# Performance work log

Hardware: AMD Instinct MI355X
Metric: run time of the kernel (lower is better)

Reference implementation:

```python
import jax, jax.numpy as jnp
import numpy as np

N, S, D, H = 4, 2048, 1024, 16
DH = D // H  # 64


def setup_inputs() -> dict:
    key = jax.random.key(0)
    ks = jax.random.split(key, 7)
    return {
        "sequences": jax.random.normal(ks[0], (N, S, D), dtype=jnp.float32),
        "Wq": jax.random.normal(ks[1], (H, DH, DH), dtype=jnp.float32) * (1.0 / np.sqrt(DH)),
        "bq": jax.random.normal(ks[2], (H, DH), dtype=jnp.float32) * 0.02,
        "Wk": jax.random.normal(ks[3], (H, DH, DH), dtype=jnp.float32) * (1.0 / np.sqrt(DH)),
        "bk": jax.random.normal(ks[4], (H, DH), dtype=jnp.float32) * 0.02,
        "Wv": jax.random.normal(ks[5], (H, DH, DH), dtype=jnp.float32) * (1.0 / np.sqrt(DH)),
        "bv": jax.random.normal(ks[6], (H, DH), dtype=jnp.float32) * 0.02,
    }


def reference(sequences, Wq, bq, Wk, bk, Wv, bv):
    n, s, d = sequences.shape
    # Each head h only sees its own slice of the embedding (block-diagonal proj)
    x = sequences.reshape(n, s, H, DH)  # (N, S, H, DH)
    q = jnp.einsum('nshd,hde->nshe', x, Wq) + bq  # (N, S, H, DH)
    k = jnp.einsum('nshd,hde->nshe', x, Wk) + bk
    v = jnp.einsum('nshd,hde->nshe', x, Wv) + bv
    scores = jnp.einsum('nqhd,nkhd->nhqk', q, k) / jnp.sqrt(jnp.float32(DH))
    attn = jax.nn.softmax(scores, axis=-1)  # (N, H, S, S)
    out = jnp.einsum('nhqk,nkhd->nqhd', attn, v)  # (N, S, H, DH)
    return out.reshape(n, s, d)  # hstack of heads == concat on last dim
```

## Files before the change

kernel.cpp:

```cpp
#include <hip/hip_runtime.h>
#include <hip/hip_bf16.h>

#define NB 4
#define SLEN 2048
#define DMODEL 1024
#define NH 16
#define DH 64

using f32x4  = __attribute__((ext_vector_type(4))) float;
using f32x8  = __attribute__((ext_vector_type(8))) float;
using f32x16 = __attribute__((ext_vector_type(16))) float;
using bf16x8 = __attribute__((ext_vector_type(8))) short;
using u32x4  = __attribute__((ext_vector_type(4))) unsigned int;

__device__ __forceinline__ unsigned short f2bf(float f) {
    unsigned int u = __float_as_uint(f);
    u += 0x7FFFu + ((u >> 16) & 1u);
    return (unsigned short)(u >> 16);
}

__device__ __forceinline__ float fast_exp2(float x) {
    float r;
    asm("v_exp_f32 %0, %1" : "=v"(r) : "v"(x));
    return r;
}

__device__ __forceinline__ unsigned cvtpk(float lo, float hi) {
    unsigned r;
    asm("v_cvt_pk_bf16_f32 %0, %1, %2" : "=v"(r) : "v"(lo), "v"(hi));
    return r;
}

__device__ __forceinline__ void permswap(unsigned& a, unsigned& b) {
    asm("v_permlane32_swap_b32 %0, %1" : "+v"(a), "+v"(b));
}

#define QSCALE 0.18033688011112042f

__global__ __launch_bounds__(256) void qkv_proj_kernel(
    const float* __restrict__ seq,
    const float* __restrict__ Wq, const float* __restrict__ bq,
    const float* __restrict__ Wk, const float* __restrict__ bk,
    const float* __restrict__ Wv, const float* __restrict__ bv,
    unsigned short* __restrict__ Qb,
    unsigned short* __restrict__ Kb,
    unsigned short* __restrict__ Vt)
{
    const int bid  = blockIdx.x;
    const int nh   = bid >> 5;
    const int tile = bid & 31;
    const int h = nh & 15;
    const int n = nh >> 4;
    const int t0 = tile * 64;
    const int tid = threadIdx.x;
    const int w  = tid >> 6;
    const int l  = tid & 63;
    const int g  = l >> 4;
    const int ln = l & 15;

    __shared__ unsigned short wt[3][64 * 72];

    {
        const float* Wsrc0 = Wq + h * 4096;
        const float* Wsrc1 = Wk + h * 4096;
        const float* Wsrc2 = Wv + h * 4096;
        for (int idx = tid; idx < 4096; idx += 256) {
            int d = idx >> 6, e = idx & 63;
            wt[0][e * 72 + d] = f2bf(Wsrc0[idx]);
            wt[1][e * 72 + d] = f2bf(Wsrc1[idx]);
            wt[2][e * 72 + d] = f2bf(Wsrc2[idx]);
        }
    }
    __syncthreads();

    const float* xrow = seq + ((size_t)(n * SLEN + t0 + w * 16 + ln)) * DMODEL + h * DH;
    bf16x8 a[2];
#pragma unroll
    for (int kk = 0; kk < 2; ++kk) {
        const float4* src = reinterpret_cast<const float4*>(xrow + kk * 32 + g * 8);
        float4 v0 = src[0];
        float4 v1 = src[1];
        bf16x8 av;
        av[0] = (short)f2bf(v0.x); av[1] = (short)f2bf(v0.y);
        av[2] = (short)f2bf(v0.z); av[3] = (short)f2bf(v0.w);
        av[4] = (short)f2bf(v1.x); av[5] = (short)f2bf(v1.y);
        av[6] = (short)f2bf(v1.z); av[7] = (short)f2bf(v1.w);
        a[kk] = av;
    }

    const float* bias0 = bq + h * DH;
    const float* bias1 = bk + h * DH;
    const float* bias2 = bv + h * DH;

#pragma unroll
    for (int p = 0; p < 3; ++p) {
#pragma unroll
        for (int cb = 0; cb < 4; ++cb) {
            f32x4 acc = {0.f, 0.f, 0.f, 0.f};
#pragma unroll
            for (int kk = 0; kk < 2; ++kk) {
                bf16x8 b = *reinterpret_cast<bf16x8*>(
                    &wt[p][(cb * 16 + ln) * 72 + kk * 32 + g * 8]);
                acc = __builtin_amdgcn_mfma_f32_16x16x32_bf16(a[kk], b, acc, 0, 0, 0);
            }
            const int col = cb * 16 + ln;
            if (p == 0) {
                const float bb = bias0[col];
#pragma unroll
                for (int r = 0; r < 4; ++r) {
                    float qv = (acc[r] + bb) * QSCALE;
                    Qb[((size_t)(nh * SLEN + t0 + w * 16 + g * 4 + r)) * DH + col] = f2bf(qv);
                }
            } else if (p == 1) {
                const float bb = bias1[col];
#pragma unroll
                for (int r = 0; r < 4; ++r) {
                    Kb[((size_t)(nh * SLEN + t0 + w * 16 + g * 4 + r)) * DH + col] =
                        f2bf(acc[r] + bb);
                }
            } else {
                const float bb = bias2[col];
                ushort4 pack;
                pack.x = f2bf(acc[0] + bb);
                pack.y = f2bf(acc[1] + bb);
                pack.z = f2bf(acc[2] + bb);
                pack.w = f2bf(acc[3] + bb);
                *reinterpret_cast<ushort4*>(
                    &Vt[((size_t)(nh * 64 + col)) * SLEN + t0 + w * 16 + g * 4]) = pack;
            }
        }
    }
}

__global__ __launch_bounds__(256) void attn_kernel(
    const unsigned short* __restrict__ Qb,
    const unsigned short* __restrict__ Kb,
    const unsigned short* __restrict__ Vt,
    float* __restrict__ out)
{
    const int bid = blockIdx.x;
    const int swz = (bid & 7) * 128 + (bid >> 3);
    const int nh = swz >> 4;
    const int qt = swz & 15;
    const int n = nh >> 4, h = nh & 15;
    const int tid = threadIdx.x;
    const int w  = tid >> 6;
    const int l  = tid & 63;
    const int lq = l & 31;
    const int hi = l >> 5;
    const int q0 = qt * 128 + w * 32;

    __shared__ unsigned short k_lds[2][64 * 64];
    __shared__ unsigned short v_lds[2][64 * 64];

    const int c_row = tid >> 3;
    const int c_sub = tid & 7;
    const int wslot = (c_sub ^ (c_row & 7)) * 8;
    const int wi0 = c_row * 64 + wslot;
    const int wi1 = wi0 + 32 * 64;

    const unsigned short* Kh = Kb + (size_t)nh * SLEN * DH;
    const unsigned short* Vh = Vt + (size_t)nh * DH * SLEN;
    const unsigned short* KgA = Kh + (size_t)c_row * DH + c_sub * 8;
    const unsigned short* KgB = KgA + (size_t)32 * DH;
    const unsigned short* VgA = Vh + (size_t)c_row * SLEN + c_sub * 8;
    const unsigned short* VgB = VgA + (size_t)32 * SLEN;

    const unsigned short* qrow = Qb + ((size_t)(nh * SLEN + q0 + lq)) * DH + hi * 8;
    bf16x8 qf[4];
#pragma unroll
    for (int ks = 0; ks < 4; ++ks)
        qf[ks] = *reinterpret_cast<const bf16x8*>(qrow + ks * 16);

    f32x16 oA, oB;
    f32x8 lacc;
#pragma unroll
    for (int r = 0; r < 16; ++r) { oA[r] = 0.f; oB[r] = 0.f; }
#pragma unroll
    for (int r = 0; r < 8; ++r) lacc[r] = 0.f;

    {
        bf16x8 kr0 = *reinterpret_cast<const bf16x8*>(KgA);
        bf16x8 kr1 = *reinterpret_cast<const bf16x8*>(KgB);
        bf16x8 vr0 = *reinterpret_cast<const bf16x8*>(VgA);
        bf16x8 vr1 = *reinterpret_cast<const bf16x8*>(VgB);
        *reinterpret_cast<bf16x8*>(&k_lds[0][wi0]) = kr0;
        *reinterpret_cast<bf16x8*>(&k_lds[0][wi1]) = kr1;
        *reinterpret_cast<bf16x8*>(&v_lds[0][wi0]) = vr0;
        *reinterpret_cast<bf16x8*>(&v_lds[0][wi1]) = vr1;
    }
    __syncthreads();

    const int rx = lq & 7;
    int cur = 0;

    for (int kt = 0; kt < SLEN; kt += 64) {
        const int ktn = (kt + 64) & (SLEN - 1);

        bf16x8 kr0 = *reinterpret_cast<const bf16x8*>(KgA + (size_t)ktn * DH);
        bf16x8 kr1 = *reinterpret_cast<const bf16x8*>(KgB + (size_t)ktn * DH);
        bf16x8 vr0 = *reinterpret_cast<const bf16x8*>(VgA + ktn);
        bf16x8 vr1 = *reinterpret_cast<const bf16x8*>(VgB + ktn);

        const unsigned short* kb0 = &k_lds[cur][0];
        const unsigned short* vb0 = &v_lds[cur][0];

        f32x16 s0, s1;
#pragma unroll
        for (int r = 0; r < 16; ++r) { s0[r] = 0.f; s1[r] = 0.f; }
        {
            bf16x8 kfA[4];
#pragma unroll
            for (int ks = 0; ks < 4; ++ks) {
                const int slot = (((ks * 2 + hi) ^ rx)) * 8;
                kfA[ks] = *reinterpret_cast<const bf16x8*>(&kb0[lq * 64 + slot]);
            }
            __builtin_amdgcn_s_setprio(1);
#pragma unroll
            for (int ks = 0; ks < 4; ++ks)
                s0 = __builtin_amdgcn_mfma_f32_32x32x16_bf16(kfA[ks], qf[ks], s0, 0, 0, 0);
            __builtin_amdgcn_s_setprio(0);
        }
        {
            bf16x8 kfB[4];
#pragma unroll
            for (int ks = 0; ks < 4; ++ks) {
                const int slot = (((ks * 2 + hi) ^ rx)) * 8;
                kfB[ks] = *reinterpret_cast<const bf16x8*>(&kb0[(lq + 32) * 64 + slot]);
            }
            __builtin_amdgcn_s_setprio(1);
#pragma unroll
            for (int ks = 0; ks < 4; ++ks)
                s1 = __builtin_amdgcn_mfma_f32_32x32x16_bf16(kfB[ks], qf[ks], s1, 0, 0, 0);
            __builtin_amdgcn_s_setprio(0);
        }

#pragma unroll
        for (int r = 0; r < 16; ++r) {
            s0[r] = fast_exp2(s0[r]);
            s1[r] = fast_exp2(s1[r]);
        }
#pragma unroll
        for (int r = 0; r < 8; ++r)
            lacc[r] += (s0[r] + s0[r + 8]) + (s1[r] + s1[r + 8]);

        bf16x8 pa0[2], pa1[2];
#pragma unroll
        for (int f = 0; f < 2; ++f) {
            const int b = f * 8;
            unsigned a0 = cvtpk(s0[b + 0], s0[b + 1]);
            unsigned b0 = cvtpk(s0[b + 4], s0[b + 5]);
            permswap(a0, b0);
            unsigned a1 = cvtpk(s0[b + 2], s0[b + 3]);
            unsigned b1 = cvtpk(s0[b + 6], s0[b + 7]);
            permswap(a1, b1);
            u32x4 t0v = {a0, a1, b0, b1};
            pa0[f] = __builtin_bit_cast(bf16x8, t0v);

            unsigned c0 = cvtpk(s1[b + 0], s1[b + 1]);
            unsigned d0 = cvtpk(s1[b + 4], s1[b + 5]);
            permswap(c0, d0);
            unsigned c1 = cvtpk(s1[b + 2], s1[b + 3]);
            unsigned d1 = cvtpk(s1[b + 6], s1[b + 7]);
            permswap(c1, d1);
            u32x4 t1v = {c0, c1, d0, d1};
            pa1[f] = __builtin_bit_cast(bf16x8, t1v);
        }

        {
            bf16x8 vfA[4], vfB[4];
#pragma unroll
            for (int f = 0; f < 4; ++f) {
                const int slot = (((f * 2 + hi) ^ rx)) * 8;
                vfA[f] = *reinterpret_cast<const bf16x8*>(&vb0[lq * 64 + slot]);
                vfB[f] = *reinterpret_cast<const bf16x8*>(&vb0[(lq + 32) * 64 + slot]);
            }
            __builtin_amdgcn_s_setprio(1);
#pragma unroll
            for (int f = 0; f < 2; ++f) {
                oA = __builtin_amdgcn_mfma_f32_32x32x16_bf16(vfA[f],     pa0[f], oA, 0, 0, 0);
                oB = __builtin_amdgcn_mfma_f32_32x32x16_bf16(vfB[f],     pa0[f], oB, 0, 0, 0);
                oA = __builtin_amdgcn_mfma_f32_32x32x16_bf16(vfA[f + 2], pa1[f], oA, 0, 0, 0);
                oB = __builtin_amdgcn_mfma_f32_32x32x16_bf16(vfB[f + 2], pa1[f], oB, 0, 0, 0);
            }
            __builtin_amdgcn_s_setprio(0);
        }

        if (ktn != 0) {
            *reinterpret_cast<bf16x8*>(&k_lds[cur ^ 1][wi0]) = kr0;
            *reinterpret_cast<bf16x8*>(&k_lds[cur ^ 1][wi1]) = kr1;
            *reinterpret_cast<bf16x8*>(&v_lds[cur ^ 1][wi0]) = vr0;
            *reinterpret_cast<bf16x8*>(&v_lds[cur ^ 1][wi1]) = vr1;
            __syncthreads();
            cur ^= 1;
        }
    }

    float lsum = ((lacc[0] + lacc[1]) + (lacc[2] + lacc[3]))
               + ((lacc[4] + lacc[5]) + (lacc[6] + lacc[7]));
    lsum += __shfl_xor(lsum, 32);

    const float inv = 1.0f / lsum;
    float* dst = out + ((size_t)(n * SLEN + q0 + lq)) * DMODEL + h * DH;
#pragma unroll
    for (int grp = 0; grp < 4; ++grp) {
        float4 stA, stB;
        stA.x = oA[4 * grp + 0] * inv; stA.y = oA[4 * grp + 1] * inv;
        stA.z = oA[4 * grp + 2] * inv; stA.w = oA[4 * grp + 3] * inv;
        stB.x = oB[4 * grp + 0] * inv; stB.y = oB[4 * grp + 1] * inv;
        stB.z = oB[4 * grp + 2] * inv; stB.w = oB[4 * grp + 3] * inv;
        *reinterpret_cast<float4*>(dst + grp * 8 + hi * 4)      = stA;
        *reinterpret_cast<float4*>(dst + 32 + grp * 8 + hi * 4) = stB;
    }
}

extern "C" void kernel_launch(void* const* d_in, const int* in_sizes, int n_in,
                              void* d_out, int out_size, void* d_ws, size_t ws_size,
                              hipStream_t stream) {
    const float* seq = (const float*)d_in[0];
    const float* Wq  = (const float*)d_in[1];
    const float* bq  = (const float*)d_in[2];
    const float* Wk  = (const float*)d_in[3];
    const float* bk  = (const float*)d_in[4];
    const float* Wv  = (const float*)d_in[5];
    const float* bv  = (const float*)d_in[6];

    const size_t per_tensor = (size_t)NB * NH * SLEN * DH;
    unsigned short* Qb = (unsigned short*)d_ws;
    unsigned short* Kb = Qb + per_tensor;
    unsigned short* Vt = Kb + per_tensor;

    qkv_proj_kernel<<<dim3(NB * NH * (SLEN / 64)), dim3(256), 0, stream>>>(
        seq, Wq, bq, Wk, bk, Wv, bv, Qb, Kb, Vt);
    attn_kernel<<<dim3(NB * NH * (SLEN / 128)), dim3(256), 0, stream>>>(
        Qb, Kb, Vt, (float*)d_out);
}
```

Baseline: 127.6 us.

## Process two 32-row query tiles per wave to reuse K/V LDS fragments

Each wave now handles 64 query rows instead of 32, so the K and V fragments read from LDS are reused across two query sub-tiles. The block covers 256 queries and the grid is halved. This cuts LDS read traffic and K/V global loads per unit of work. The LDS swizzle also gains an extra XOR term to reduce bank conflicts. In exchange, register pressure roughly doubles from four output accumulators and four score tiles, which may lower occupancy, and the smaller grid of 512 blocks may underfill the CUs.

```diff
diff --git a/kernel.cpp b/kernel.cpp
--- a/kernel.cpp
+++ b/kernel.cpp
@@ -8,7 +8,6 @@
 #define DH 64
 
 using f32x4  = __attribute__((ext_vector_type(4))) float;
-using f32x8  = __attribute__((ext_vector_type(8))) float;
 using f32x16 = __attribute__((ext_vector_type(16))) float;
 using bf16x8 = __attribute__((ext_vector_type(8))) short;
 using u32x4  = __attribute__((ext_vector_type(4))) unsigned int;
@@ -139,25 +138,25 @@
     float* __restrict__ out)
 {
     const int bid = blockIdx.x;
-    const int swz = (bid & 7) * 128 + (bid >> 3);
-    const int nh = swz >> 4;
-    const int qt = swz & 15;
+    const int swz = (bid & 7) * 64 + (bid >> 3);
+    const int nh = swz >> 3;
+    const int qt = swz & 7;
     const int n = nh >> 4, h = nh & 15;
     const int tid = threadIdx.x;
     const int w  = tid >> 6;
     const int l  = tid & 63;
     const int lq = l & 31;
     const int hi = l >> 5;
-    const int q0 = qt * 128 + w * 32;
+    const int wq0 = qt * 256 + w * 64;
 
     __shared__ unsigned short k_lds[2][64 * 64];
     __shared__ unsigned short v_lds[2][64 * 64];
 
     const int c_row = tid >> 3;
     const int c_sub = tid & 7;
-    const int wslot = (c_sub ^ (c_row & 7)) * 8;
-    const int wi0 = c_row * 64 + wslot;
-    const int wi1 = wi0 + 32 * 64;
+    const int ws0 = ((c_sub ^ (c_row & 7) ^ (c_row >> 3)) & 7) * 8;
+    const int wi0 = c_row * 64 + ws0;
+    const int wi1 = (c_row + 32) * 64 + (ws0 ^ 32);
 
     const unsigned short* Kh = Kb + (size_t)nh * SLEN * DH;
     const unsigned short* Vh = Vt + (size_t)nh * DH * SLEN;
@@ -166,18 +165,20 @@
     const unsigned short* VgA = Vh + (size_t)c_row * SLEN + c_sub * 8;
     const unsigned short* VgB = VgA + (size_t)32 * SLEN;
 
-    const unsigned short* qrow = Qb + ((size_t)(nh * SLEN + q0 + lq)) * DH + hi * 8;
-    bf16x8 qf[4];
-#pragma unroll
-    for (int ks = 0; ks < 4; ++ks)
-        qf[ks] = *reinterpret_cast<const bf16x8*>(qrow + ks * 16);
-
-    f32x16 oA, oB;
-    f32x8 lacc;
-#pragma unroll
-    for (int r = 0; r < 16; ++r) { oA[r] = 0.f; oB[r] = 0.f; }
-#pragma unroll
-    for (int r = 0; r < 8; ++r) lacc[r] = 0.f;
+    const unsigned short* qrow = Qb + ((size_t)(nh * SLEN + wq0 + lq)) * DH + hi * 8;
+    bf16x8 qf0[4], qf1[4];
+#pragma unroll
+    for (int ks = 0; ks < 4; ++ks) {
+        qf0[ks] = *reinterpret_cast<const bf16x8*>(qrow + ks * 16);
+        qf1[ks] = *reinterpret_cast<const bf16x8*>(qrow + (size_t)32 * DH + ks * 16);
+    }
+
+    f32x16 oA0, oB0, oA1, oB1;
+    f32x4 lacc0, lacc1;
+#pragma unroll
+    for (int r = 0; r < 16; ++r) { oA0[r] = 0.f; oB0[r] = 0.f; oA1[r] = 0.f; oB1[r] = 0.f; }
+#pragma unroll
+    for (int r = 0; r < 4; ++r) { lacc0[r] = 0.f; lacc1[r] = 0.f; }
 
     {
         bf16x8 kr0 = *reinterpret_cast<const bf16x8*>(KgA);
@@ -191,7 +192,7 @@
     }
     __syncthreads();
 
-    const int rx = lq & 7;
+    const int rxg = (lq & 7) ^ (lq >> 3);
     int cur = 0;
 
     for (int kt = 0; kt < SLEN; kt += 64) {
@@ -205,83 +206,112 @@
         const unsigned short* kb0 = &k_lds[cur][0];
         const unsigned short* vb0 = &v_lds[cur][0];
 
-        f32x16 s0, s1;
-#pragma unroll
-        for (int r = 0; r < 16; ++r) { s0[r] = 0.f; s1[r] = 0.f; }
+        bf16x8 kfA[4], kfB[4];
+#pragma unroll
+        for (int ks = 0; ks < 4; ++ks) {
+            const int slot = (((ks * 2 + hi) ^ rxg) & 7) * 8;
+            kfA[ks] = *reinterpret_cast<const bf16x8*>(&kb0[lq * 64 + slot]);
+            kfB[ks] = *reinterpret_cast<const bf16x8*>(&kb0[(lq + 32) * 64 + (slot ^ 32)]);
+        }
+
+        f32x16 sA0, sA1, sB0, sB1;
+#pragma unroll
+        for (int r = 0; r < 16; ++r) { sA0[r] = 0.f; sA1[r] = 0.f; sB0[r] = 0.f; sB1[r] = 0.f; }
+        __builtin_amdgcn_s_setprio(1);
+#pragma unroll
+        for (int ks = 0; ks < 4; ++ks) {
+            sA0 = __builtin_amdgcn_mfma_f32_32x32x16_bf16(kfA[ks], qf0[ks], sA0, 0, 0, 0);
+            sB0 = __builtin_amdgcn_mfma_f32_32x32x16_bf16(kfA[ks], qf1[ks], sB0, 0, 0, 0);
+        }
+#pragma unroll
+        for (int ks = 0; ks < 4; ++ks) {
+            sA1 = __builtin_amdgcn_mfma_f32_32x32x16_bf16(kfB[ks], qf0[ks], sA1, 0, 0, 0);
+            sB1 = __builtin_amdgcn_mfma_f32_32x32x16_bf16(kfB[ks], qf1[ks], sB1, 0, 0, 0);
+        }
+        __builtin_amdgcn_s_setprio(0);
+
+        bf16x8 paA0[2], paA1[2], paB0[2], paB1[2];
+#pragma unroll
+        for (int r = 0; r < 16; ++r) {
+            sA0[r] = fast_exp2(sA0[r]);
+            sA1[r] = fast_exp2(sA1[r]);
+        }
+#pragma unroll
+        for (int r = 0; r < 4; ++r)
+            lacc0[r] += ((sA0[r] + sA0[r + 4]) + (sA0[r + 8] + sA0[r + 12]))
+                      + ((sA1[r] + sA1[r + 4]) + (sA1[r + 8] + sA1[r + 12]));
+#pragma unroll
+        for (int f = 0; f < 2; ++f) {
+            const int b = f * 8;
+            unsigned a0 = cvtpk(sA0[b + 0], sA0[b + 1]);
+            unsigned b0 = cvtpk(sA0[b + 4], sA0[b + 5]);
+            permswap(a0, b0);
+            unsigned a1 = cvtpk(sA0[b + 2], sA0[b + 3]);
+            unsigned b1 = cvtpk(sA0[b + 6], sA0[b + 7]);
+            permswap(a1, b1);
+            u32x4 t0v = {a0, a1, b0, b1};
+            paA0[f] = __builtin_bit_cast(bf16x8, t0v);
+
+            unsigned c0 = cvtpk(sA1[b + 0], sA1[b + 1]);
+            unsigned d0 = cvtpk(sA1[b + 4], sA1[b + 5]);
+            permswap(c0, d0);
+            unsigned c1 = cvtpk(sA1[b + 2], sA1[b + 3]);
+            unsigned d1 = cvtpk(sA1[b + 6], sA1[b + 7]);
+            permswap(c1, d1);
+            u32x4 t1v = {c0, c1, d0, d1};
+            paA1[f] = __builtin_bit_cast(bf16x8, t1v);
+        }
+
+#pragma unroll
+        for (int r = 0; r < 16; ++r) {
+            sB0[r] = fast_exp2(sB0[r]);
+            sB1[r] = fast_exp2(sB1[r]);
+        }
+#pragma unroll
+        for (int r = 0; r < 4; ++r)
+            lacc1[r] += ((sB0[r] + sB0[r + 4]) + (sB0[r + 8] + sB0[r + 12]))
+                      + ((sB1[r] + sB1[r + 4]) + (sB1[r + 8] + sB1[r + 12]));
+#pragma unroll
+        for (int f = 0; f < 2; ++f) {
+            const int b = f * 8;
+            unsigned a0 = cvtpk(sB0[b + 0], sB0[b + 1]);
+            unsigned b0 = cvtpk(sB0[b + 4], sB0[b + 5]);
+            permswap(a0, b0);
+            unsigned a1 = cvtpk(sB0[b + 2], sB0[b + 3]);
+            unsigned b1 = cvtpk(sB0[b + 6], sB0[b + 7]);
+            permswap(a1, b1);
+            u32x4 t0v = {a0, a1, b0, b1};
+            paB0[f] = __builtin_bit_cast(bf16x8, t0v);
+
+            unsigned c0 = cvtpk(sB1[b + 0], sB1[b + 1]);
+            unsigned d0 = cvtpk(sB1[b + 4], sB1[b + 5]);
+            permswap(c0, d0);
+            unsigned c1 = cvtpk(sB1[b + 2], sB1[b + 3]);
+            unsigned d1 = cvtpk(sB1[b + 6], sB1[b + 7]);
+            permswap(c1, d1);
+            u32x4 t1v = {c0, c1, d0, d1};
+            paB1[f] = __builtin_bit_cast(bf16x8, t1v);
+        }
+
         {
-            bf16x8 kfA[4];
-#pragma unroll
-            for (int ks = 0; ks < 4; ++ks) {
-                const int slot = (((ks * 2 + hi) ^ rx)) * 8;
-                kfA[ks] = *reinterpret_cast<const bf16x8*>(&kb0[lq * 64 + slot]);
+            bf16x8 vfA[4], vfB[4];
+#pragma unroll
+            for (int f = 0; f < 4; ++f) {
+                const int slot = (((f * 2 + hi) ^ rxg) & 7) * 8;
+                vfA[f] = *reinterpret_cast<const bf16x8*>(&vb0[lq * 64 + slot]);
+                vfB[f] = *reinterpret_cast<const bf16x8*>(&vb0[(lq + 32) * 64 + (slot ^ 32)]);
             }
             __builtin_amdgcn_s_setprio(1);
 #pragma unroll
-            for (int ks = 0; ks < 4; ++ks)
-                s0 = __builtin_amdgcn_mfma_f32_32x32x16_bf16(kfA[ks], qf[ks], s0, 0, 0, 0);
-            __builtin_amdgcn_s_setprio(0);
-        }
-        {
-            bf16x8 kfB[4];
-#pragma unroll
-            for (int ks = 0; ks < 4; ++ks) {
-                const int slot = (((ks * 2 + hi) ^ rx)) * 8;
-                kfB[ks] = *reinterpret_cast<const bf16x8*>(&kb0[(lq + 32) * 64 + slot]);
-            }
-            __builtin_amdgcn_s_setprio(1);
-#pragma unroll
-            for (int ks = 0; ks < 4; ++ks)
-                s1 = __builtin_amdgcn_mfma_f32_32x32x16_bf16(kfB[ks], qf[ks], s1, 0, 0, 0);
-            __builtin_amdgcn_s_setprio(0);
-        }
-
-#pragma unroll
-        for (int r = 0; r < 16; ++r) {
-            s0[r] = fast_exp2(s0[r]);
-            s1[r] = fast_exp2(s1[r]);
-        }
-#pragma unroll
-        for (int r = 0; r < 8; ++r)
-            lacc[r] += (s0[r] + s0[r + 8]) + (s1[r] + s1[r + 8]);
-
-        bf16x8 pa0[2], pa1[2];
-#pragma unroll
-        for (int f = 0; f < 2; ++f) {
-            const int b = f * 8;
-            unsigned a0 = cvtpk(s0[b + 0], s0[b + 1]);
-            unsigned b0 = cvtpk(s0[b + 4], s0[b + 5]);
-            permswap(a0, b0);
-            unsigned a1 = cvtpk(s0[b + 2], s0[b + 3]);
-            unsigned b1 = cvtpk(s0[b + 6], s0[b + 7]);
-            permswap(a1, b1);
-            u32x4 t0v = {a0, a1, b0, b1};
-            pa0[f] = __builtin_bit_cast(bf16x8, t0v);
-
-            unsigned c0 = cvtpk(s1[b + 0], s1[b + 1]);
-            unsigned d0 = cvtpk(s1[b + 4], s1[b + 5]);
-            permswap(c0, d0);
-            unsigned c1 = cvtpk(s1[b + 2], s1[b + 3]);
-            unsigned d1 = cvtpk(s1[b + 6], s1[b + 7]);
-            permswap(c1, d1);
-            u32x4 t1v = {c0, c1, d0, d1};
-            pa1[f] = __builtin_bit_cast(bf16x8, t1v);
-        }
-
-        {
-            bf16x8 vfA[4], vfB[4];
-#pragma unroll
-            for (int f = 0; f < 4; ++f) {
-                const int slot = (((f * 2 + hi) ^ rx)) * 8;
-                vfA[f] = *reinterpret_cast<const bf16x8*>(&vb0[lq * 64 + slot]);
-                vfB[f] = *reinterpret_cast<const bf16x8*>(&vb0[(lq + 32) * 64 + slot]);
-            }
-            __builtin_amdgcn_s_setprio(1);
-#pragma unroll
             for (int f = 0; f < 2; ++f) {
-                oA = __builtin_amdgcn_mfma_f32_32x32x16_bf16(vfA[f],     pa0[f], oA, 0, 0, 0);
-                oB = __builtin_amdgcn_mfma_f32_32x32x16_bf16(vfB[f],     pa0[f], oB, 0, 0, 0);
-                oA = __builtin_amdgcn_mfma_f32_32x32x16_bf16(vfA[f + 2], pa1[f], oA, 0, 0, 0);
-                oB = __builtin_amdgcn_mfma_f32_32x32x16_bf16(vfB[f + 2], pa1[f], oB, 0, 0, 0);
+                oA0 = __builtin_amdgcn_mfma_f32_32x32x16_bf16(vfA[f],     paA0[f], oA0, 0, 0, 0);
+                oB0 = __builtin_amdgcn_mfma_f32_32x32x16_bf16(vfB[f],     paA0[f], oB0, 0, 0, 0);
+                oA0 = __builtin_amdgcn_mfma_f32_32x32x16_bf16(vfA[f + 2], paA1[f], oA0, 0, 0, 0);
+                oB0 = __builtin_amdgcn_mfma_f32_32x32x16_bf16(vfB[f + 2], paA1[f], oB0, 0, 0, 0);
+                oA1 = __builtin_amdgcn_mfma_f32_32x32x16_bf16(vfA[f],     paB0[f], oA1, 0, 0, 0);
+                oB1 = __builtin_amdgcn_mfma_f32_32x32x16_bf16(vfB[f],     paB0[f], oB1, 0, 0, 0);
+                oA1 = __builtin_amdgcn_mfma_f32_32x32x16_bf16(vfA[f + 2], paB1[f], oA1, 0, 0, 0);
+                oB1 = __builtin_amdgcn_mfma_f32_32x32x16_bf16(vfB[f + 2], paB1[f], oB1, 0, 0, 0);
             }
             __builtin_amdgcn_s_setprio(0);
         }
@@ -296,21 +326,30 @@
         }
     }
 
-    float lsum = ((lacc[0] + lacc[1]) + (lacc[2] + lacc[3]))
-               + ((lacc[4] + lacc[5]) + (lacc[6] + lacc[7]));
-    lsum += __shfl_xor(lsum, 32);
-
-    const float inv = 1.0f / lsum;
-    float* dst = out + ((size_t)(n * SLEN + q0 + lq)) * DMODEL + h * DH;
+    float lsum0 = (lacc0[0] + lacc0[1]) + (lacc0[2] + lacc0[3]);
+    lsum0 += __shfl_xor(lsum0, 32);
+    float lsum1 = (lacc1[0] + lacc1[1]) + (lacc1[2] + lacc1[3]);
+    lsum1 += __shfl_xor(lsum1, 32);
+
+    const float inv0 = 1.0f / lsum0;
+    const float inv1 = 1.0f / lsum1;
+    float* dst0 = out + ((size_t)(n * SLEN + wq0 + lq)) * DMODEL + h * DH;
+    float* dst1 = dst0 + (size_t)32 * DMODEL;
 #pragma unroll
     for (int grp = 0; grp < 4; ++grp) {
-        float4 stA, stB;
-        stA.x = oA[4 * grp + 0] * inv; stA.y = oA[4 * grp + 1] * inv;
-        stA.z = oA[4 * grp + 2] * inv; stA.w = oA[4 * grp + 3] * inv;
-        stB.x = oB[4 * grp + 0] * inv; stB.y = oB[4 * grp + 1] * inv;
-        stB.z = oB[4 * grp + 2] * inv; stB.w = oB[4 * grp + 3] * inv;
-        *reinterpret_cast<float4*>(dst + grp * 8 + hi * 4)      = stA;
-        *reinterpret_cast<float4*>(dst + 32 + grp * 8 + hi * 4) = stB;
+        float4 st;
+        st.x = oA0[4 * grp + 0] * inv0; st.y = oA0[4 * grp + 1] * inv0;
+        st.z = oA0[4 * grp + 2] * inv0; st.w = oA0[4 * grp + 3] * inv0;
+        *reinterpret_cast<float4*>(dst0 + grp * 8 + hi * 4) = st;
+        st.x = oB0[4 * grp + 0] * inv0; st.y = oB0[4 * grp + 1] * inv0;
+        st.z = oB0[4 * grp + 2] * inv0; st.w = oB0[4 * grp + 3] * inv0;
+        *reinterpret_cast<float4*>(dst0 + 32 + grp * 8 + hi * 4) = st;
+        st.x = oA1[4 * grp + 0] * inv1; st.y = oA1[4 * grp + 1] * inv1;
+        st.z = oA1[4 * grp + 2] * inv1; st.w = oA1[4 * grp + 3] * inv1;
+        *reinterpret_cast<float4*>(dst1 + grp * 8 + hi * 4) = st;
+        st.x = oB1[4 * grp + 0] * inv1; st.y = oB1[4 * grp + 1] * inv1;
+        st.z = oB1[4 * grp + 2] * inv1; st.w = oB1[4 * grp + 3] * inv1;
+        *reinterpret_cast<float4*>(dst1 + 32 + grp * 8 + hi * 4) = st;
     }
 }
 
@@ -332,6 +371,6 @@
 
     qkv_proj_kernel<<<dim3(NB * NH * (SLEN / 64)), dim3(256), 0, stream>>>(
         seq, Wq, bq, Wk, bk, Wv, bv, Qb, Kb, Vt);
-    attn_kernel<<<dim3(NB * NH * (SLEN / 128)), dim3(256), 0, stream>>>(
+    attn_kernel<<<dim3(NB * NH * (SLEN / 256)), dim3(256), 0, stream>>>(
         Qb, Kb, Vt, (float*)d_out);
 }
```

After: 151.7 us. 18.9% more time.
